# Kernel optimization log

Hardware: AMD Instinct MI355X
Metric: run time of the kernel (lower is better)

## Reference

```python
import jax, jax.numpy as jnp
import numpy as np

H, DK = 8, 64  # n_head, d_k (= d_v)
LN_EPS = 1e-6


def _layer_norm(x, g, b):
    mu = jnp.mean(x, axis=-1, keepdims=True)
    var = jnp.var(x, axis=-1, keepdims=True)
    return (x - mu) * jax.lax.rsqrt(var + LN_EPS) * g + b


def setup_inputs() -> dict:
    key = jax.random.key(0)
    ks = jax.random.split(key, 8)
    B, S, D, DF = 8, 1024, 512, 2048
    s = 0.02
    return {
        "enc_input": jax.random.normal(ks[0], (B, S, D), jnp.float32),
        "cost_mat": jax.random.normal(ks[1], (B, S, S), jnp.float32),
        "wq": jax.random.normal(ks[2], (D, D), jnp.float32) * s,
        "wk": jax.random.normal(ks[3], (D, D), jnp.float32) * s,
        "wv": jax.random.normal(ks[4], (D, D), jnp.float32) * s,
        "fc_w": jax.random.normal(ks[5], (D, D), jnp.float32) * s,
        "ln1_g": jnp.ones((D,), jnp.float32),
        "ln1_b": jnp.zeros((D,), jnp.float32),
        "w1": jax.random.normal(ks[6], (DF, D), jnp.float32) * s,
        "b1": jnp.zeros((DF,), jnp.float32),
        "w2": jax.random.normal(ks[7], (D, DF), jnp.float32) * s,
        "b2": jnp.zeros((D,), jnp.float32),
        "ln2_g": jnp.ones((D,), jnp.float32),
        "ln2_b": jnp.zeros((D,), jnp.float32),
    }


def reference(enc_input, cost_mat, wq, wk, wv, fc_w, ln1_g, ln1_b,
              w1, b1, w2, b2, ln2_g, ln2_b):
    B, S, D = enc_input.shape
    # Q/K/V projections -> [B, H, S, dk]
    q = (enc_input @ wq.T).reshape(B, S, H, DK).transpose(0, 2, 1, 3)
    k = (enc_input @ wk.T).reshape(B, S, H, DK).transpose(0, 2, 1, 3)
    v = (enc_input @ wv.T).reshape(B, S, H, DK).transpose(0, 2, 1, 3)
    # mixed score: scaled QK^T plus cost matrix broadcast over heads
    scores = jnp.einsum("bhqd,bhkd->bhqk", q, k) / np.sqrt(DK).astype(np.float32)
    scores = scores + cost_mat[:, None, :, :]
    attn = jax.nn.softmax(scores, axis=-1)
    ctx = jnp.einsum("bhqk,bhkd->bhqd", attn, v)  # [B,H,S,dk]
    ctx = ctx.transpose(0, 2, 1, 3).reshape(B, S, D)
    attn_out = _layer_norm(ctx @ fc_w.T + enc_input, ln1_g, ln1_b)
    # position-wise FFN with residual + layernorm
    h = jax.nn.relu(attn_out @ w1.T + b1)
    ffn = h @ w2.T + b2
    return _layer_norm(ffn + attn_out, ln2_g, ln2_b)
```

## Files before the change

kernel.cpp:

```cpp
#include <hip/hip_runtime.h>
#include <stdint.h>

typedef __attribute__((ext_vector_type(8))) short bf16x8;
typedef __attribute__((ext_vector_type(4))) float f32x4;

__device__ __forceinline__ unsigned short f2bf(float f) {
  unsigned int u = __builtin_bit_cast(unsigned int, f);
  u += 0x7fffu + ((u >> 16) & 1u);
  return (unsigned short)(u >> 16);
}

__device__ __forceinline__ float bf2f(unsigned short u) {
  unsigned int x = ((unsigned int)u) << 16;
  return __builtin_bit_cast(float, x);
}

__device__ __forceinline__ void gload16(const void* g, void* l) {
  __builtin_amdgcn_global_load_lds(
      (const __attribute__((address_space(1))) void*)g,
      (__attribute__((address_space(3))) void*)l, 16, 0, 0);
}

__global__ void cvt_all(const float* __restrict__ enc,
                        const float* __restrict__ cost,
                        const float* __restrict__ wq,
                        const float* __restrict__ wk,
                        const float* __restrict__ wv,
                        const float* __restrict__ fcw,
                        const float* __restrict__ w1,
                        const float* __restrict__ w2,
                        unsigned short* __restrict__ enc_bf,
                        unsigned short* __restrict__ cost_bf,
                        unsigned short* __restrict__ wqkv_bf,
                        unsigned short* __restrict__ fcw_bf,
                        unsigned short* __restrict__ w1_bf,
                        unsigned short* __restrict__ w2_bf) {
  const int i = blockIdx.x * 256 + threadIdx.x;
  constexpr int E0 = 1048576;
  constexpr int E1 = E0 + 2097152;
  constexpr int E2 = E1 + 65536;
  constexpr int E3 = E2 + 65536;
  constexpr int E4 = E3 + 65536;
  constexpr int E5 = E4 + 65536;
  constexpr int E6 = E5 + 262144;
  constexpr int E7 = E6 + 262144;
  const float* in;
  unsigned short* out;
  int base;
  float scale = 1.0f;
  if (i < E0)      { in = enc;  out = enc_bf;            base = 0;  }
  else if (i < E1) { in = cost; out = cost_bf;           base = E0; scale = 1.44269504f; }
  else if (i < E2) { in = wq;   out = wqkv_bf;           base = E1; }
  else if (i < E3) { in = wk;   out = wqkv_bf + 262144;  base = E2; }
  else if (i < E4) { in = wv;   out = wqkv_bf + 524288;  base = E3; }
  else if (i < E5) { in = fcw;  out = fcw_bf;            base = E4; }
  else if (i < E6) { in = w1;   out = w1_bf;             base = E5; }
  else if (i < E7) { in = w2;   out = w2_bf;             base = E6; }
  else return;
  const int k = i - base;
  float4 v = ((const float4*)in)[k];
  ushort4 o;
  o.x = f2bf(v.x * scale);
  o.y = f2bf(v.y * scale);
  o.z = f2bf(v.z * scale);
  o.w = f2bf(v.w * scale);
  ((ushort4*)out)[k] = o;
}

template <int EPI>
__global__ __launch_bounds__(256, 2) void gemm_bt(
    const unsigned short* __restrict__ A, const unsigned short* __restrict__ B,
    void* __restrict__ C, const float* __restrict__ bias, int M, int N, int K) {
  __shared__ unsigned short Al[2][128 * 32];
  __shared__ unsigned short Bl[2][128 * 32];
  const int tid = threadIdx.x;
  const int lane = tid & 63;
  const int wid = tid >> 6;
  const int wr = wid >> 1;
  const int wc = wid & 1;
  const int m0 = blockIdx.y * 128;
  const int n0 = blockIdx.x * 128;

  f32x4 acc[4][4];
#pragma unroll
  for (int i = 0; i < 4; ++i)
#pragma unroll
    for (int j = 0; j < 4; ++j) acc[i][j] = f32x4{0.f, 0.f, 0.f, 0.f};

  const int srow = wid * 32 + (lane >> 2);
  const int scol = (lane & 3) * 8;
  const unsigned short* Ag = A + (size_t)(m0 + srow) * K + scol;
  const unsigned short* Bg = B + (size_t)(n0 + srow) * K + scol;
  const size_t K16 = (size_t)16 * K;

  auto stage = [&](int buf, int kt) {
    unsigned short* Ald = &Al[buf][wid * 1024];
    unsigned short* Bld = &Bl[buf][wid * 1024];
    gload16(Ag + kt, Ald);
    gload16(Ag + K16 + kt, Ald + 512);
    gload16(Bg + kt, Bld);
    gload16(Bg + K16 + kt, Bld + 512);
  };

  const int ko = (lane >> 4) * 8;
  const int arow = wr * 64 + (lane & 15);
  const int brow = wc * 64 + (lane & 15);

  stage(0, 0);
  __syncthreads();
  for (int kt = 0, it = 0; kt < K; kt += 32, ++it) {
    const int cur = it & 1;
    if (kt + 32 < K) stage(cur ^ 1, kt + 32);
    bf16x8 af[4], bf[4];
#pragma unroll
    for (int mi = 0; mi < 4; ++mi)
      af[mi] = *(const bf16x8*)&Al[cur][(arow + mi * 16) * 32 + ko];
#pragma unroll
    for (int ni = 0; ni < 4; ++ni)
      bf[ni] = *(const bf16x8*)&Bl[cur][(brow + ni * 16) * 32 + ko];
#pragma unroll
    for (int mi = 0; mi < 4; ++mi)
#pragma unroll
      for (int ni = 0; ni < 4; ++ni)
        acc[mi][ni] = __builtin_amdgcn_mfma_f32_16x16x32_bf16(
            af[mi], bf[ni], acc[mi][ni], 0, 0, 0);
    __syncthreads();
  }

  const int rl = (lane >> 4) * 4;
  const int cl = lane & 15;
#pragma unroll
  for (int mi = 0; mi < 4; ++mi) {
#pragma unroll
    for (int ni = 0; ni < 4; ++ni) {
      const int r0 = m0 + wr * 64 + mi * 16 + rl;
      const int c = n0 + wc * 64 + ni * 16 + cl;
      if (EPI == 5 && c >= 1024) {
        unsigned short* Vt = (unsigned short*)C + (size_t)2 * 8192 * 512;
        const int cc = c - 1024;
        ushort4 pk;
        pk.x = f2bf(acc[mi][ni][0]);
        pk.y = f2bf(acc[mi][ni][1]);
        pk.z = f2bf(acc[mi][ni][2]);
        pk.w = f2bf(acc[mi][ni][3]);
        const int b_ = r0 >> 10, s_ = r0 & 1023, h_ = cc >> 6, dd = cc & 63;
        *(ushort4*)(Vt + ((size_t)((b_ * 8 + h_) * 64 + dd) * 1024 + s_)) = pk;
      } else if (EPI == 5) {
        unsigned short* dst =
            (c < 512) ? (unsigned short*)C + (size_t)r0 * 512 + c
                      : (unsigned short*)C + (size_t)8192 * 512 +
                            (size_t)r0 * 512 + (c - 512);
#pragma unroll
        for (int j = 0; j < 4; ++j) dst[(size_t)j * 512] = f2bf(acc[mi][ni][j]);
      } else {
#pragma unroll
        for (int j = 0; j < 4; ++j) {
          float v = acc[mi][ni][j];
          if (EPI == 2 || EPI == 6) v += bias[c];
          if (EPI == 2) v = fmaxf(v, 0.f);
          ((unsigned short*)C)[(size_t)(r0 + j) * N + c] = f2bf(v);
        }
      }
    }
  }
}

template <int EPI>
__global__ __launch_bounds__(256, 2) void gemm_bt64(
    const unsigned short* __restrict__ A, const unsigned short* __restrict__ B,
    void* __restrict__ C, const float* __restrict__ bias, int M, int N, int K) {
  __shared__ unsigned short Al[2][64 * 32];
  __shared__ unsigned short Bl[2][128 * 32];
  const int tid = threadIdx.x;
  const int lane = tid & 63;
  const int wid = tid >> 6;
  const int m0 = blockIdx.y * 64;
  const int n0 = blockIdx.x * 128;

  f32x4 acc[4][2];
#pragma unroll
  for (int i = 0; i < 4; ++i)
#pragma unroll
    for (int j = 0; j < 2; ++j) acc[i][j] = f32x4{0.f, 0.f, 0.f, 0.f};

  const int srow = tid >> 2;
  const int scol = (tid & 3) * 8;
  const unsigned short* Ag = A + (size_t)(m0 + srow) * K + scol;
  const unsigned short* Bg = B + (size_t)(n0 + srow) * K + scol;
  const size_t K64 = (size_t)64 * K;

  auto stage = [&](int buf, int kt) {
    gload16(Ag + kt, &Al[buf][wid * 512]);
    gload16(Bg + kt, &Bl[buf][wid * 512]);
    gload16(Bg + K64 + kt, &Bl[buf][2048 + wid * 512]);
  };

  const int ko = (lane >> 4) * 8;
  const int cl16 = lane & 15;

  stage(0, 0);
  __syncthreads();
  for (int kt = 0, it = 0; kt < K; kt += 32, ++it) {
    const int cur = it & 1;
    if (kt + 32 < K) stage(cur ^ 1, kt + 32);
    bf16x8 af[4], bf[2];
#pragma unroll
    for (int mi = 0; mi < 4; ++mi)
      af[mi] = *(const bf16x8*)&Al[cur][(mi * 16 + cl16) * 32 + ko];
#pragma unroll
    for (int ni = 0; ni < 2; ++ni)
      bf[ni] = *(const bf16x8*)&Bl[cur][(wid * 32 + ni * 16 + cl16) * 32 + ko];
#pragma unroll
    for (int mi = 0; mi < 4; ++mi)
#pragma unroll
      for (int ni = 0; ni < 2; ++ni)
        acc[mi][ni] = __builtin_amdgcn_mfma_f32_16x16x32_bf16(
            af[mi], bf[ni], acc[mi][ni], 0, 0, 0);
    __syncthreads();
  }

  const int rl = (lane >> 4) * 4;
#pragma unroll
  for (int mi = 0; mi < 4; ++mi) {
#pragma unroll
    for (int ni = 0; ni < 2; ++ni) {
      const int r0 = m0 + mi * 16 + rl;
      const int c = n0 + wid * 32 + ni * 16 + cl16;
#pragma unroll
      for (int j = 0; j < 4; ++j) {
        float v = acc[mi][ni][j];
        if (EPI == 6) v += bias[c];
        ((unsigned short*)C)[(size_t)(r0 + j) * N + c] = f2bf(v);
      }
    }
  }
}

__global__ __launch_bounds__(512, 4) void attn_kernel(
    const unsigned short* __restrict__ Q, const unsigned short* __restrict__ K,
    const unsigned short* __restrict__ V,
    const unsigned short* __restrict__ Cb,
    unsigned short* __restrict__ ctx) {
  __shared__ unsigned short Kl[2][4096];
  __shared__ unsigned short Vl[2][4096];
  __shared__ unsigned short Cl[8192];
  __shared__ unsigned short P[8][16 * 84];
  const int tid = threadIdx.x, lane = tid & 63, wid = tid >> 6;
  const int bh = blockIdx.y, b = bh >> 3, h = bh & 7;
  const int q0 = blockIdx.x * 128;
  const int qw = q0 + wid * 16;
  const int cl = lane & 15, gl = lane >> 4;

  const unsigned short* qp =
      Q + (size_t)(b * 1024 + qw + cl) * 512 + h * 64 + gl * 8;
  const bf16x8 qf0 = *(const bf16x8*)qp;
  const bf16x8 qf1 = *(const bf16x8*)(qp + 32);

  f32x4 acc[4];
  float lsum[4];
#pragma unroll
  for (int i = 0; i < 4; ++i) {
    acc[i] = f32x4{0.f, 0.f, 0.f, 0.f};
    lsum[i] = 0.f;
  }

  const int srow = tid >> 3;
  const int swzc = ((tid & 7) * 8) ^ ((srow & 7) << 3);
  const unsigned short* Ksrc =
      K + (size_t)(b * 1024 + srow) * 512 + h * 64 + swzc;
  const unsigned short* Vsrc = V + (size_t)(bh * 64 + srow) * 1024 + swzc;
  const unsigned short* Csrc =
      Cb + (size_t)(b * 1024 + q0 + srow) * 1024 + swzc;

  auto stage_kv = [&](int buf, int k0) {
    gload16(Ksrc + (size_t)k0 * 512, &Kl[buf][wid * 512]);
    gload16(Vsrc + k0, &Vl[buf][wid * 512]);
  };
  auto stage_c = [&](int k0) {
    gload16(Csrc + k0, &Cl[wid * 512]);
    gload16(Csrc + (size_t)64 * 1024 + k0, &Cl[4096 + wid * 512]);
  };

  const int ks = (cl & 7) << 3;

  stage_kv(0, 0);
  stage_c(0);
  __syncthreads();

  for (int t = 0; t < 16; ++t) {
    const int cur = t & 1;
    if (t < 15) stage_kv(cur ^ 1, (t + 1) * 64);

#pragma unroll
    for (int ni = 0; ni < 4; ++ni) {
      const int krow = ni * 16 + cl;
      bf16x8 k0f = *(const bf16x8*)&Kl[cur][krow * 64 + ((gl * 8) ^ ks)];
      bf16x8 k1f = *(const bf16x8*)&Kl[cur][krow * 64 + ((32 + gl * 8) ^ ks)];
      f32x4 t2 = f32x4{0.f, 0.f, 0.f, 0.f};
      t2 = __builtin_amdgcn_mfma_f32_16x16x32_bf16(qf0, k0f, t2, 0, 0, 0);
      t2 = __builtin_amdgcn_mfma_f32_16x16x32_bf16(qf1, k1f, t2, 0, 0, 0);
#pragma unroll
      for (int j = 0; j < 4; ++j) {
        const int qrow = wid * 16 + gl * 4 + j;
        const float cf =
            bf2f(Cl[qrow * 64 + ((ni * 16 + cl) ^ ((qrow & 7) << 3))]);
        const float ex = __builtin_fmaf(t2[j], 0.18033688f, cf);
        float p;
        asm("v_exp_f32 %0, %1" : "=v"(p) : "v"(ex));
        lsum[j] += p;
        P[wid][(gl * 4 + j) * 84 + ni * 16 + cl] = f2bf(p);
      }
    }
    __builtin_amdgcn_sched_barrier(0);
    __builtin_amdgcn_s_barrier();
    __builtin_amdgcn_sched_barrier(0);
    if (t < 15) stage_c((t + 1) * 64);

    bf16x8 pf0 = *(const bf16x8*)&P[wid][cl * 84 + gl * 8];
    bf16x8 pf1 = *(const bf16x8*)&P[wid][cl * 84 + 32 + gl * 8];
#pragma unroll
    for (int nv = 0; nv < 4; ++nv) {
      const int vrow = nv * 16 + cl;
      bf16x8 v0f = *(const bf16x8*)&Vl[cur][vrow * 64 + ((gl * 8) ^ ks)];
      bf16x8 v1f = *(const bf16x8*)&Vl[cur][vrow * 64 + ((32 + gl * 8) ^ ks)];
      acc[nv] =
          __builtin_amdgcn_mfma_f32_16x16x32_bf16(pf0, v0f, acc[nv], 0, 0, 0);
      acc[nv] =
          __builtin_amdgcn_mfma_f32_16x16x32_bf16(pf1, v1f, acc[nv], 0, 0, 0);
    }
    __syncthreads();
  }

  float linv[4];
#pragma unroll
  for (int j = 0; j < 4; ++j) {
    float r = lsum[j];
    r += __shfl_xor(r, 1);
    r += __shfl_xor(r, 2);
    r += __shfl_xor(r, 4);
    r += __shfl_xor(r, 8);
    linv[j] = 1.0f / r;
  }
#pragma unroll
  for (int nv = 0; nv < 4; ++nv)
#pragma unroll
    for (int j = 0; j < 4; ++j) {
      float v = acc[nv][j] * linv[j];
      ctx[(size_t)(b * 1024 + qw + gl * 4 + j) * 512 + h * 64 + nv * 16 + cl] =
          f2bf(v);
    }
}

template <int OUT_F32>
__global__ __launch_bounds__(256) void ln_kernel(
    const unsigned short* __restrict__ x1, const unsigned short* __restrict__ x2,
    const float* __restrict__ g, const float* __restrict__ bt,
    void* __restrict__ out) {
  const int lane = threadIdx.x & 63, wid = threadIdx.x >> 6;
  const int row = blockIdx.x * 4 + wid;
  const bf16x8 a = *(const bf16x8*)(x1 + (size_t)row * 512 + lane * 8);
  const bf16x8 bb = *(const bf16x8*)(x2 + (size_t)row * 512 + lane * 8);
  float x[8];
#pragma unroll
  for (int i = 0; i < 8; ++i)
    x[i] = bf2f((unsigned short)a[i]) + bf2f((unsigned short)bb[i]);
  float sum = 0.f, sq = 0.f;
#pragma unroll
  for (int i = 0; i < 8; ++i) {
    sum += x[i];
    sq += x[i] * x[i];
  }
#pragma unroll
  for (int m = 1; m <= 32; m <<= 1) {
    sum += __shfl_xor(sum, m);
    sq += __shfl_xor(sq, m);
  }
  const float mean = sum * (1.f / 512.f);
  const float var = sq * (1.f / 512.f) - mean * mean;
  const float rstd = rsqrtf(var + 1e-6f);
  float y[8];
#pragma unroll
  for (int i = 0; i < 8; ++i) {
    const int c = lane * 8 + i;
    y[i] = (x[i] - mean) * rstd * g[c] + bt[c];
  }
  if (OUT_F32) {
    float4* op = (float4*)((float*)out + (size_t)row * 512);
    op[lane * 2] = make_float4(y[0], y[1], y[2], y[3]);
    op[lane * 2 + 1] = make_float4(y[4], y[5], y[6], y[7]);
  } else {
    bf16x8 o;
#pragma unroll
    for (int i = 0; i < 8; ++i) o[i] = (short)f2bf(y[i]);
    *(bf16x8*)((unsigned short*)out + (size_t)row * 512 + lane * 8) = o;
  }
}

extern "C" void kernel_launch(void* const* d_in, const int* in_sizes, int n_in,
                              void* d_out, int out_size, void* d_ws,
                              size_t ws_size, hipStream_t stream) {
  const float* enc = (const float*)d_in[0];
  const float* cost = (const float*)d_in[1];
  const float* wq = (const float*)d_in[2];
  const float* wk = (const float*)d_in[3];
  const float* wv = (const float*)d_in[4];
  const float* fcw = (const float*)d_in[5];
  const float* ln1g = (const float*)d_in[6];
  const float* ln1b = (const float*)d_in[7];
  const float* w1 = (const float*)d_in[8];
  const float* b1 = (const float*)d_in[9];
  const float* w2 = (const float*)d_in[10];
  const float* b2 = (const float*)d_in[11];
  const float* ln2g = (const float*)d_in[12];
  const float* ln2b = (const float*)d_in[13];

  char* ws = (char*)d_ws;
  size_t off = 0;
  auto alloc = [&](size_t n) {
    void* p = ws + off;
    off += (n + 255) & ~(size_t)255;
    return p;
  };
  const size_t MD = 8192ull * 512;
  const size_t MF = 8192ull * 2048;
  unsigned short* enc_bf = (unsigned short*)alloc(MD * 2);
  unsigned short* wqkv_bf = (unsigned short*)alloc(3 * 512 * 512 * 2);
  unsigned short* fcw_bf = (unsigned short*)alloc(512 * 512 * 2);
  unsigned short* w1_bf = (unsigned short*)alloc(2048 * 512 * 2);
  unsigned short* w2_bf = (unsigned short*)alloc(512 * 2048 * 2);
  unsigned short* Qb = (unsigned short*)alloc(MD * 2 * 3);
  unsigned short* Kb = Qb + MD;
  unsigned short* Vt = Kb + MD;
  unsigned short* ctx_bf = (unsigned short*)alloc(MD * 2);
  unsigned short* fc_bf = (unsigned short*)alloc(MD * 2);
  unsigned short* attn_bf = (unsigned short*)alloc(MD * 2);
  unsigned short* ffn_bf = (unsigned short*)alloc(MD * 2);
  unsigned short* h_bf = (unsigned short*)alloc(MF * 2);
  unsigned short* cost_bf = h_bf;

  cvt_all<<<15360, 256, 0, stream>>>(enc, cost, wq, wk, wv, fcw, w1, w2,
                                     enc_bf, cost_bf, wqkv_bf, fcw_bf, w1_bf,
                                     w2_bf);

  gemm_bt<5><<<dim3(12, 64), 256, 0, stream>>>(enc_bf, wqkv_bf, Qb, nullptr,
                                               8192, 1536, 512);
  attn_kernel<<<dim3(8, 64), 512, 0, stream>>>(Qb, Kb, Vt, cost_bf, ctx_bf);
  gemm_bt64<0><<<dim3(4, 128), 256, 0, stream>>>(ctx_bf, fcw_bf, fc_bf,
                                                 nullptr, 8192, 512, 512);
  ln_kernel<0><<<2048, 256, 0, stream>>>(fc_bf, enc_bf, ln1g, ln1b, attn_bf);
  gemm_bt<2><<<dim3(16, 64), 256, 0, stream>>>(attn_bf, w1_bf, h_bf, b1, 8192,
                                               2048, 512);
  gemm_bt64<6><<<dim3(4, 128), 256, 0, stream>>>(h_bf, w2_bf, ffn_bf, b2, 8192,
                                                 512, 2048);
  ln_kernel<1><<<2048, 256, 0, stream>>>(ffn_bf, attn_bf, ln2g, ln2b, d_out);
}
```

Before: 164.4 us.

## Transpose QK^T MFMA so each lane owns one query row for vectorized softmax

Swaps the MFMA operand order so the score tile comes out transposed, with each lane holding four consecutive keys of one query row. The cost-matrix read becomes a single 8-byte LDS load instead of four scalar loads, and P is written with packed bf16 conversion and one 8-byte store into an XOR-swizzled 64-wide layout instead of four scalar stores into a padded layout. The row-sum reduction is simplified to a single per-lane accumulator, followed by a shuffle redistribution at the end. It relies on the swizzle being consistent between the P writes and the PV reads.

```diff
diff --git a/kernel.cpp b/kernel.cpp
--- a/kernel.cpp
+++ b/kernel.cpp
@@ -244,7 +244,7 @@
   __shared__ unsigned short Kl[2][4096];
   __shared__ unsigned short Vl[2][4096];
   __shared__ unsigned short Cl[8192];
-  __shared__ unsigned short P[8][16 * 84];
+  __shared__ unsigned short P[8][1024];
   const int tid = threadIdx.x, lane = tid & 63, wid = tid >> 6;
   const int bh = blockIdx.y, b = bh >> 3, h = bh & 7;
   const int q0 = blockIdx.x * 128;
@@ -257,12 +257,9 @@
   const bf16x8 qf1 = *(const bf16x8*)(qp + 32);
 
   f32x4 acc[4];
-  float lsum[4];
-#pragma unroll
-  for (int i = 0; i < 4; ++i) {
-    acc[i] = f32x4{0.f, 0.f, 0.f, 0.f};
-    lsum[i] = 0.f;
-  }
+  float lsum = 0.f;
+#pragma unroll
+  for (int i = 0; i < 4; ++i) acc[i] = f32x4{0.f, 0.f, 0.f, 0.f};
 
   const int srow = tid >> 3;
   const int swzc = ((tid & 7) * 8) ^ ((srow & 7) << 3);
@@ -282,6 +279,8 @@
   };
 
   const int ks = (cl & 7) << 3;
+  const int pswz = (cl & 7) << 3;
+  const int crow = wid * 16 + cl;
 
   stage_kv(0, 0);
   stage_c(0);
@@ -297,27 +296,33 @@
       bf16x8 k0f = *(const bf16x8*)&Kl[cur][krow * 64 + ((gl * 8) ^ ks)];
       bf16x8 k1f = *(const bf16x8*)&Kl[cur][krow * 64 + ((32 + gl * 8) ^ ks)];
       f32x4 t2 = f32x4{0.f, 0.f, 0.f, 0.f};
-      t2 = __builtin_amdgcn_mfma_f32_16x16x32_bf16(qf0, k0f, t2, 0, 0, 0);
-      t2 = __builtin_amdgcn_mfma_f32_16x16x32_bf16(qf1, k1f, t2, 0, 0, 0);
-#pragma unroll
-      for (int j = 0; j < 4; ++j) {
-        const int qrow = wid * 16 + gl * 4 + j;
-        const float cf =
-            bf2f(Cl[qrow * 64 + ((ni * 16 + cl) ^ ((qrow & 7) << 3))]);
-        const float ex = __builtin_fmaf(t2[j], 0.18033688f, cf);
-        float p;
-        asm("v_exp_f32 %0, %1" : "=v"(p) : "v"(ex));
-        lsum[j] += p;
-        P[wid][(gl * 4 + j) * 84 + ni * 16 + cl] = f2bf(p);
+      t2 = __builtin_amdgcn_mfma_f32_16x16x32_bf16(k0f, qf0, t2, 0, 0, 0);
+      t2 = __builtin_amdgcn_mfma_f32_16x16x32_bf16(k1f, qf1, t2, 0, 0, 0);
+      const uint2 cpk = *(const uint2*)&Cl[crow * 64 + ((ni * 16 + gl * 4) ^ pswz)];
+      float p0, p1, p2, p3;
+      {
+        float e0 = __builtin_fmaf(t2[0], 0.18033688f, bf2f((unsigned short)(cpk.x & 0xffff)));
+        float e1 = __builtin_fmaf(t2[1], 0.18033688f, bf2f((unsigned short)(cpk.x >> 16)));
+        float e2 = __builtin_fmaf(t2[2], 0.18033688f, bf2f((unsigned short)(cpk.y & 0xffff)));
+        float e3 = __builtin_fmaf(t2[3], 0.18033688f, bf2f((unsigned short)(cpk.y >> 16)));
+        asm("v_exp_f32 %0, %1" : "=v"(p0) : "v"(e0));
+        asm("v_exp_f32 %0, %1" : "=v"(p1) : "v"(e1));
+        asm("v_exp_f32 %0, %1" : "=v"(p2) : "v"(e2));
+        asm("v_exp_f32 %0, %1" : "=v"(p3) : "v"(e3));
       }
+      lsum += (p0 + p1) + (p2 + p3);
+      uint32_t lo, hi;
+      asm("v_cvt_pk_bf16_f32 %0, %1, %2" : "=v"(lo) : "v"(p0), "v"(p1));
+      asm("v_cvt_pk_bf16_f32 %0, %1, %2" : "=v"(hi) : "v"(p2), "v"(p3));
+      *(uint2*)&P[wid][cl * 64 + ((ni * 16 + gl * 4) ^ pswz)] = uint2{lo, hi};
     }
     __builtin_amdgcn_sched_barrier(0);
     __builtin_amdgcn_s_barrier();
     __builtin_amdgcn_sched_barrier(0);
     if (t < 15) stage_c((t + 1) * 64);
 
-    bf16x8 pf0 = *(const bf16x8*)&P[wid][cl * 84 + gl * 8];
-    bf16x8 pf1 = *(const bf16x8*)&P[wid][cl * 84 + 32 + gl * 8];
+    bf16x8 pf0 = *(const bf16x8*)&P[wid][cl * 64 + ((gl * 8) ^ pswz)];
+    bf16x8 pf1 = *(const bf16x8*)&P[wid][cl * 64 + ((32 + gl * 8) ^ pswz)];
 #pragma unroll
     for (int nv = 0; nv < 4; ++nv) {
       const int vrow = nv * 16 + cl;
@@ -331,21 +336,17 @@
     __syncthreads();
   }
 
-  float linv[4];
-#pragma unroll
-  for (int j = 0; j < 4; ++j) {
-    float r = lsum[j];
-    r += __shfl_xor(r, 1);
-    r += __shfl_xor(r, 2);
-    r += __shfl_xor(r, 4);
-    r += __shfl_xor(r, 8);
-    linv[j] = 1.0f / r;
-  }
+  lsum += __shfl_xor(lsum, 16);
+  lsum += __shfl_xor(lsum, 32);
+  const float linv = 1.0f / lsum;
+  float linvw[4];
+#pragma unroll
+  for (int j = 0; j < 4; ++j) linvw[j] = __shfl(linv, gl * 4 + j);
 #pragma unroll
   for (int nv = 0; nv < 4; ++nv)
 #pragma unroll
     for (int j = 0; j < 4; ++j) {
-      float v = acc[nv][j] * linv[j];
+      float v = acc[nv][j] * linvw[j];
       ctx[(size_t)(b * 1024 + qw + gl * 4 + j) * 512 + h * 64 + nv * 16 + cl] =
           f2bf(v);
     }
```

Result: faster. 159.6 us (-2.9%).
